# Kernel tuning notes

Hardware: AMD Instinct MI355X
Metric: run time of the kernel (lower is better)

Reference implementation:

```python
import jax, jax.numpy as jnp
import numpy as np

C, CL = 64, 8
N_PTS, GRID = 250_000, 160
G2 = GRID // 2


def _build():
    """Build sparse coords and MinkowskiEngine-style kernel maps (numpy, int constants)."""
    rng = np.random.default_rng(0)
    raw = rng.integers(0, GRID, size=(int(N_PTS * 1.3), 3))
    keys = (raw[:, 0] * GRID + raw[:, 1]) * GRID + raw[:, 2]
    _, uidx = np.unique(keys, return_index=True)
    coords = raw[np.sort(uidx)][:N_PTS]
    n_in = coords.shape[0]
    # conv1: kernel 2, stride 2 -> each input voxel maps to exactly one output via one of 8 offsets
    down = coords // 2
    dkeys = (down[:, 0] * G2 + down[:, 1]) * G2 + down[:, 2]
    ukeys, inv = np.unique(dkeys, return_inverse=True)
    n_out = int(ukeys.shape[0])
    kid = (coords[:, 0] % 2) * 4 + (coords[:, 1] % 2) * 2 + (coords[:, 2] % 2)
    lists = [np.where(kid == k)[0] for k in range(8)]
    M1 = max(len(l) for l in lists)
    in1 = np.full((8, M1), n_in, np.int32)   # pad -> zero feature row
    out1 = np.full((8, M1), n_out, np.int32)  # pad -> dropped output row
    for k, l in enumerate(lists):
        in1[k, :len(l)] = l
        out1[k, :len(l)] = inv[l]
    # kernel-3, stride-1 map on the downsampled coordinate set (27 offsets)
    D = np.stack([ukeys // (G2 * G2), (ukeys // G2) % G2, ukeys % G2], 1)
    offs = [(a, b, c) for a in (-1, 0, 1) for b in (-1, 0, 1) for c in (-1, 0, 1)]
    pin, pout = [], []
    for o in offs:
        nd = D + np.array(o)
        valid = np.all((nd >= 0) & (nd < G2), 1)
        nk = (nd[:, 0] * G2 + nd[:, 1]) * G2 + nd[:, 2]
        pos = np.minimum(np.searchsorted(ukeys, nk), n_out - 1)
        found = valid & (ukeys[pos] == nk)
        ii = np.where(found)[0]
        pin.append(ii)
        pout.append(pos[ii])
    M3 = max(len(p) for p in pin)
    in3 = np.full((27, M3), n_out, np.int32)
    out3 = np.full((27, M3), n_out, np.int32)
    for k in range(27):
        in3[k, :len(pin[k])] = pin[k]
        out3[k, :len(pin[k])] = pout[k]
    return n_in, n_out, in1, out1, in3, out3


def setup_inputs() -> dict:
    n_in, n_out, in1, out1, in3, out3 = _build()
    key = jax.random.key(0)
    ks = jax.random.split(key, 16)
    s = 0.05
    return dict(
        x_F=jax.random.normal(ks[0], (n_in, C), jnp.float32),
        ctx_F=jax.random.normal(ks[1], (n_in, C), jnp.float32),
        W1=jax.random.normal(ks[2], (8, 2 * C, C), jnp.float32) * s,
        b1=jax.random.normal(ks[3], (C,), jnp.float32) * s,
        Wr00=jax.random.normal(ks[4], (27, C, C // 4), jnp.float32) * s,
        br00=jax.random.normal(ks[5], (C // 4,), jnp.float32) * s,
        Wr01=jax.random.normal(ks[6], (27, C // 4, C // 2), jnp.float32) * s,
        br01=jax.random.normal(ks[7], (C // 2,), jnp.float32) * s,
        Wr10=jax.random.normal(ks[8], (C, C // 4), jnp.float32) * s,
        br10=jax.random.normal(ks[9], (C // 4,), jnp.float32) * s,
        Wr11=jax.random.normal(ks[10], (27, C // 4, C // 4), jnp.float32) * s,
        br11=jax.random.normal(ks[11], (C // 4,), jnp.float32) * s,
        Wr12=jax.random.normal(ks[12], (C // 4, C // 2), jnp.float32) * s,
        br12=jax.random.normal(ks[13], (C // 2,), jnp.float32) * s,
        W2=jax.random.normal(ks[14], (27, C, CL), jnp.float32) * s,
        b2=jax.random.normal(ks[15], (CL,), jnp.float32) * s,
        in1=jnp.asarray(in1), out1=jnp.asarray(out1),
        in3=jnp.asarray(in3), out3=jnp.asarray(out3),
        n_out=n_out,
    )


def _sconv(F, W, b, in_idx, out_idx, n_out):
    """Kernel-map sparse conv: per-offset gather -> GEMM -> scatter-add. F:[N,Cin], W:[K,Cin,Cout]."""
    Fp = jnp.concatenate([F, jnp.zeros((1, F.shape[1]), F.dtype)], 0)
    y = jnp.zeros((n_out + 1, W.shape[2]), F.dtype)
    for k in range(W.shape[0]):  # fixed small kernel volume (8 or 27)
        y = y.at[out_idx[k]].add(Fp[in_idx[k]] @ W[k])
    return y[:n_out] + b


def reference(x_F, ctx_F, W1, b1, Wr00, br00, Wr01, br01, Wr10, br10, Wr11, br11, Wr12, br12, W2, b2, in1, out1, in3, out3, n_out):
    relu = jax.nn.relu
    f = jnp.concatenate([x_F, ctx_F], 1)               # cat(x.F, context1.F)
    h = _sconv(f, W1, b1, in1, out1, n_out)            # conv1: 2C->C, k=2, s=2
    # InceptionResNet block (PCGCv2-style)
    out0 = _sconv(relu(_sconv(h, Wr00, br00, in3, out3, n_out)), Wr01, br01, in3, out3, n_out)
    t = relu(h @ Wr10 + br10)                          # 1x1 conv
    t = relu(_sconv(t, Wr11, br11, in3, out3, n_out))  # 3x3 conv
    path1 = t @ Wr12 + br12                            # 1x1 conv
    h = jnp.concatenate([out0, path1], 1) + h          # cat + residual
    return _sconv(h, W2, b2, in3, out3, n_out)         # conv2: C->CL, k=3, s=1
```

## Files before the change

### kernel.cpp

```cpp
#include <hip/hip_runtime.h>

#define DEV __device__ __forceinline__

typedef __attribute__((ext_vector_type(8))) short bf16x8;
typedef __attribute__((ext_vector_type(4))) float f32x4;

DEV float4 ld4(const float* p){ return *reinterpret_cast<const float4*>(p); }

DEV unsigned short f2bf(float f){
    union { float f; unsigned u; } v; v.f = f;
    unsigned r = v.u + 0x7fffu + ((v.u >> 16) & 1u);
    return (unsigned short)(r >> 16);
}
DEV float bf2f(unsigned short s){
    union { unsigned u; float f; } v; v.u = ((unsigned)s) << 16;
    return v.f;
}

DEV void async16(const void* g, void* l){
    __builtin_amdgcn_global_load_lds(
        (const __attribute__((address_space(1))) unsigned*)g,
        (__attribute__((address_space(3))) unsigned*)l, 16, 0, 0);
}

DEV int xcd_swizzle(int orig, int nwg){
    int q = nwg >> 3, r = nwg & 7;
    int x = orig & 7, i = orig >> 3;
    return (x < r ? x*(q+1) : r*(q+1) + (x-r)*q) + i;
}

__global__ __launch_bounds__(256)
void inv_init(int* __restrict__ inv, long n, int defv){
    long i = (long)blockIdx.x*256 + threadIdx.x;
    if (i < n) inv[i] = defv;
}

__global__ __launch_bounds__(256)
void inv_build(const int* __restrict__ inK, const int* __restrict__ outK,
               int* __restrict__ inv, int M, int n_out){
    int k = blockIdx.y;
    int m = blockIdx.x*256 + threadIdx.x;
    if (m >= M) return;
    int o = outK[(long)k*M + m];
    if (o != n_out) inv[(long)k*n_out + o] = inK[(long)k*M + m];
}

__global__ __launch_bounds__(256)
void zero_rows(unsigned short* A, unsigned short* B, unsigned short* C,
               unsigned short* D, unsigned short* E, unsigned short* Z,
               int n_out, int n_in){
    int t = threadIdx.x;
    if (t < 64)       A[(long)n_out*64 + t] = 0;
    else if (t < 80)  B[(long)n_out*16 + (t-64)] = 0;
    else if (t < 144) C[(long)n_out*64 + (t-80)] = 0;
    else if (t < 160) D[(long)n_out*16 + (t-144)] = 0;
    else if (t < 176) E[(long)n_out*16 + (t-160)] = 0;
    else if (t < 240) Z[(long)n_in*64 + (t-176)] = 0;
}

__global__ __launch_bounds__(256)
void wfrag_unpaired(const float* __restrict__ W, unsigned short* __restrict__ F,
                    int KC, int NT, int CIN, int CR, int total){
    int idx = blockIdx.x*256 + threadIdx.x;
    if (idx >= total) return;
    int j = idx & 7, l = (idx >> 3) & 63, rest = idx >> 9;
    int nt = rest % NT, cc = rest / NT;
    int k = cc / KC, kc = cc % KC;
    int g = l >> 4, c = l & 15;
    int cin = kc*32 + g*8 + j, cout = nt*16 + c;
    float v = (cout < CR) ? W[((long)k*CIN + cin)*CR + cout] : 0.f;
    F[idx] = f2bf(v);
}

__global__ __launch_bounds__(256)
void wfrag_paired(const float* __restrict__ W, unsigned short* __restrict__ F,
                  int NKr, int NT, int CR, int total){
    int idx = blockIdx.x*256 + threadIdx.x;
    if (idx >= total) return;
    int j = idx & 7, l = (idx >> 3) & 63, rest = idx >> 9;
    int nt = rest % NT, cc = rest / NT;
    int g = l >> 4, c = l & 15;
    int koff = 2*cc + (g >> 1);
    int cin = (g & 1)*8 + j, cout = nt*16 + c;
    float v = (koff < NKr && cout < CR) ? W[((long)koff*16 + cin)*CR + cout] : 0.f;
    F[idx] = f2bf(v);
}

template<bool RELU, bool OUTBF16, int YS, int CR>
__global__ __launch_bounds__(256)
void gather27_lds(const void* __restrict__ Xv, const unsigned short* __restrict__ Wf,
                  const int* __restrict__ inv, const float* __restrict__ bias,
                  void* __restrict__ Yv, int n_out)
{
    __shared__ alignas(16) char buf[2*16384];
    const int lane = threadIdx.x & 63, w = threadIdx.x >> 6;
    const int bid = xcd_swizzle(blockIdx.x, gridDim.x);
    const long jblock = (long)bid * 64;
    if (jblock >= n_out) return;
    const int r = lane & 15, g = lane >> 4;
    const char* X = (const char*)Xv;
    const bf16x8* __restrict__ WF = (const bf16x8*)Wf;

    const int scol = (((lane & 7) ^ (lane >> 3)) << 4);
    const long jr0 = min(jblock + w*16 +     (lane >> 3), (long)n_out - 1);
    const long jr1 = min(jblock + w*16 + 8 + (lane >> 3), (long)n_out - 1);

    const int ro0 = w*4096 + r*128 + (( 0 + g*16) ^ ((r & 7) << 4));
    const int ro1 = w*4096 + r*128 + ((64 + g*16) ^ ((r & 7) << 4));

    f32x4 acc = {0,0,0,0};

    int i0a = inv[jr0],                 i0b = inv[jr1];
    int i1a = inv[(long)n_out + jr0],   i1b = inv[(long)n_out + jr1];
    {
        char* d = buf + w*4096;
        async16(X + (long)i0a*128 + scol, d);
        async16(X + (long)i0b*128 + scol, d + 1024);
        async16(X + (long)i1a*128 + scol, d + 2048);
        async16(X + (long)i1b*128 + scol, d + 3072);
    }
    int n0a = inv[(long)2*n_out + jr0], n0b = inv[(long)2*n_out + jr1];
    int n1a = inv[(long)3*n_out + jr0], n1b = inv[(long)3*n_out + jr1];
    bf16x8 w00 = WF[0*64 + lane], w01 = WF[1*64 + lane];
    bf16x8 w10 = WF[2*64 + lane], w11 = WF[3*64 + lane];
    __syncthreads();

    #pragma unroll 1
    for (int t = 0; t < 13; ++t){
        const int cb = t & 1;
        {
            char* d = buf + (cb^1)*16384 + w*4096;
            async16(X + (long)n0a*128 + scol, d);
            async16(X + (long)n0b*128 + scol, d + 1024);
            async16(X + (long)n1a*128 + scol, d + 2048);
            async16(X + (long)n1b*128 + scol, d + 3072);
        }
        const long kiA = (long)min(2*t+4, 26) * n_out;
        const long kiB = (long)min(2*t+5, 26) * n_out;
        int t0a = inv[kiA + jr0], t0b = inv[kiA + jr1];
        int t1a = inv[kiB + jr0], t1b = inv[kiB + jr1];
        const long kwA = (long)min(2*t+2, 26) * 2;
        const long kwB = (long)min(2*t+3, 26) * 2;
        bf16x8 nw00 = WF[(kwA  )*64 + lane], nw01 = WF[(kwA+1)*64 + lane];
        bf16x8 nw10 = WF[(kwB  )*64 + lane], nw11 = WF[(kwB+1)*64 + lane];
        const char* base = buf + cb*16384;
        bf16x8 a00 = *(const bf16x8*)(base + ro0);
        bf16x8 a01 = *(const bf16x8*)(base + ro1);
        bf16x8 a10 = *(const bf16x8*)(base + 2048 + ro0);
        bf16x8 a11 = *(const bf16x8*)(base + 2048 + ro1);
        acc = __builtin_amdgcn_mfma_f32_16x16x32_bf16(a00, w00, acc, 0, 0, 0);
        acc = __builtin_amdgcn_mfma_f32_16x16x32_bf16(a01, w01, acc, 0, 0, 0);
        acc = __builtin_amdgcn_mfma_f32_16x16x32_bf16(a10, w10, acc, 0, 0, 0);
        acc = __builtin_amdgcn_mfma_f32_16x16x32_bf16(a11, w11, acc, 0, 0, 0);
        __syncthreads();
        n0a=t0a; n0b=t0b; n1a=t1a; n1b=t1b;
        w00=nw00; w01=nw01; w10=nw10; w11=nw11;
    }
    {
        const char* base = buf + 16384;
        bf16x8 a00 = *(const bf16x8*)(base + ro0);
        bf16x8 a01 = *(const bf16x8*)(base + ro1);
        acc = __builtin_amdgcn_mfma_f32_16x16x32_bf16(a00, w00, acc, 0, 0, 0);
        acc = __builtin_amdgcn_mfma_f32_16x16x32_bf16(a01, w01, acc, 0, 0, 0);
    }

    const float bv = (r < CR) ? bias[r] : 0.f;
    #pragma unroll
    for (int q = 0; q < 4; ++q){
        long row = jblock + w*16 + g*4 + q;
        if (row < n_out){
            float v = acc[q] + bv;
            if constexpr (RELU) v = fmaxf(v, 0.f);
            if constexpr (OUTBF16) ((unsigned short*)Yv)[row*YS + r] = f2bf(v);
            else if (r < CR)       ((float*)Yv)[row*YS + r] = v;
        }
    }
}

__global__ __launch_bounds__(256, 8)
void conv1_z(const float* __restrict__ xF, const float* __restrict__ cF,
             const unsigned short* __restrict__ Wfc1, const int* __restrict__ in1,
             unsigned short* __restrict__ Z, int M1, int n_in)
{
    __shared__ unsigned short tz[4][16*64];
    const int k = blockIdx.x;
    const int lane = threadIdx.x & 63, wave = threadIdx.x >> 6;
    const int m0 = (blockIdx.y*4 + wave)*16;
    if (m0 >= M1) return;
    const int r = lane & 15, g = lane >> 4;
    const int* __restrict__ in1k = in1 + (long)k*M1;
    const int mc = min(m0 + r, M1-1);
    const int i = in1k[mc];
    const bool valid = i < n_in;
    const long iv = valid ? i : 0;
    const bf16x8* __restrict__ WF = (const bf16x8*)(Wfc1 + (size_t)k*16*512);
    const bf16x8 az = {0,0,0,0,0,0,0,0};
    f32x4 acc[4];
    #pragma unroll
    for (int nt=0; nt<4; ++nt) acc[nt] = f32x4{0,0,0,0};

    float4 lo[4], hi[4];
    #pragma unroll
    for (int kc=0; kc<4; ++kc){
        const float* s = (kc < 2) ? (xF + iv*64 + kc*32 + g*8)
                                  : (cF + iv*64 + (kc-2)*32 + g*8);
        lo[kc] = ld4(s);
        hi[kc] = ld4(s+4);
    }
    #pragma unroll
    for (int kc=0; kc<4; ++kc){
        bf16x8 a;
        a[0]=(short)f2bf(lo[kc].x); a[1]=(short)f2bf(lo[kc].y);
        a[2]=(short)f2bf(lo[kc].z); a[3]=(short)f2bf(lo[kc].w);
        a[4]=(short)f2bf(hi[kc].x); a[5]=(short)f2bf(hi[kc].y);
        a[6]=(short)f2bf(hi[kc].z); a[7]=(short)f2bf(hi[kc].w);
        if (!valid) a = az;
        #pragma unroll
        for (int nt=0; nt<4; ++nt){
            bf16x8 wv = WF[((long)kc*4 + nt)*64 + lane];
            acc[nt] = __builtin_amdgcn_mfma_f32_16x16x32_bf16(a, wv, acc[nt], 0, 0, 0);
        }
    }

    #pragma unroll
    for (int q=0; q<4; ++q)
        #pragma unroll
        for (int nt=0; nt<4; ++nt)
            tz[wave][(g*4+q)*64 + nt*16 + r] = f2bf(acc[nt][q]);
    __syncthreads();
    #pragma unroll
    for (int it=0; it<2; ++it){
        int cid = it*64 + lane;
        int row = cid >> 3, c8 = (cid & 7)*8;
        int m = m0 + row;
        if (m < M1){
            int oi = in1k[m];
            long drow = (oi < n_in) ? (long)oi : (long)n_in + 1;
            *(bf16x8*)(Z + drow*64 + c8) = *(const bf16x8*)(&tz[wave][row*64 + c8]);
        }
    }
}

__global__ __launch_bounds__(256)
void conv1_sum(const unsigned short* __restrict__ Z, const int* __restrict__ inv1,
               const float* __restrict__ b1, unsigned short* __restrict__ A, int n_out)
{
    const int bid = xcd_swizzle(blockIdx.x, gridDim.x);
    const long t = (long)bid*256 + threadIdx.x;
    const long o = t >> 3;
    if (o >= n_out) return;
    const int c8 = (int)(t & 7) * 8;
    int b[8];
    #pragma unroll
    for (int k=0;k<8;++k) b[k] = inv1[(long)k*n_out + o];
    float acc[8];
    #pragma unroll
    for (int j=0;j<2;++j){
        float4 v = ld4(b1 + c8 + 4*j);
        acc[4*j]=v.x; acc[4*j+1]=v.y; acc[4*j+2]=v.z; acc[4*j+3]=v.w;
    }
    #pragma unroll
    for (int k=0;k<8;++k){
        bf16x8 z = *(const bf16x8*)(Z + (long)b[k]*64 + c8);
        #pragma unroll
        for (int j=0;j<8;++j) acc[j] += bf2f((unsigned short)z[j]);
    }
    bf16x8 outv;
    #pragma unroll
    for (int j=0;j<8;++j) outv[j] = (short)f2bf(acc[j]);
    *(bf16x8*)(A + o*64 + c8) = outv;
}

template<int NK, int G, int NT, int RB, bool RELU, int RESBASE,
         int YS, int CB, int CR, int WPE>
__global__ __launch_bounds__(256, WPE)
void mfma_g1(const void* __restrict__ Xv, const unsigned short* __restrict__ Wf,
             const int* __restrict__ inv, const float* __restrict__ bias,
             const unsigned short* __restrict__ RES, unsigned short* __restrict__ Y, int n_out)
{
    const int lane = threadIdx.x & 63, wave = threadIdx.x >> 6;
    const int jbase = (blockIdx.x*4 + wave)*32;
    if (jbase >= n_out) return;
    const int r = lane & 15, g = lane >> 4;
    const int jc0 = min(jbase + r, n_out-1), jc1 = min(jbase + 16 + r, n_out-1);
    const char* X = (const char*)Xv;
    const bf16x8* __restrict__ WF = (const bf16x8*)Wf;
    f32x4 acc0[NT], acc1[NT];
    #pragma unroll
    for (int nt=0; nt<NT; ++nt){ acc0[nt] = f32x4{0,0,0,0}; acc1[nt] = f32x4{0,0,0,0}; }

    #pragma unroll 1
    for (int g0 = 0; g0 < NK; g0 += G) {
        int b0[G], b1[G];
        #pragma unroll
        for (int kk=0; kk<G; ++kk){
            int koff = 2*(g0+kk) + (g >> 1);
            b0[kk] = inv[(long)koff*n_out + jc0];
            b1[kk] = inv[(long)koff*n_out + jc1];
        }
        #pragma unroll
        for (int kk=0; kk<G; ++kk){
            const int k = g0 + kk;
            bf16x8 a0 = *(const bf16x8*)(X + (long)b0[kk]*RB + (g&1)*16);
            bf16x8 a1 = *(const bf16x8*)(X + (long)b1[kk]*RB + (g&1)*16);
            #pragma unroll
            for (int nt=0; nt<NT; ++nt){
                bf16x8 wv = WF[((long)k*NT + nt)*64 + lane];
                acc0[nt] = __builtin_amdgcn_mfma_f32_16x16x32_bf16(a0, wv, acc0[nt], 0, 0, 0);
                acc1[nt] = __builtin_amdgcn_mfma_f32_16x16x32_bf16(a1, wv, acc1[nt], 0, 0, 0);
            }
        }
    }

    float bi[NT];
    #pragma unroll
    for (int nt=0; nt<NT; ++nt){
        int c = nt*16 + r;
        bi[nt] = (c < CR) ? bias[c] : 0.f;
    }
    #pragma unroll
    for (int q=0; q<4; ++q){
        int row = jbase + g*4 + q;
        if (row < n_out){
            #pragma unroll
            for (int nt=0; nt<NT; ++nt){
                int c = nt*16 + r;
                float v = acc0[nt][q] + bi[nt];
                if constexpr (RESBASE >= 0) v += bf2f(RES[(long)row*64 + RESBASE + c]);
                if constexpr (RELU) v = fmaxf(v, 0.f);
                Y[(long)row*YS + CB + c] = f2bf(v);
            }
        }
        int row2 = jbase + 16 + g*4 + q;
        if (row2 < n_out){
            #pragma unroll
            for (int nt=0; nt<NT; ++nt){
                int c = nt*16 + r;
                float v = acc1[nt][q] + bi[nt];
                if constexpr (RESBASE >= 0) v += bf2f(RES[(long)row2*64 + RESBASE + c]);
                if constexpr (RELU) v = fmaxf(v, 0.f);
                Y[(long)row2*YS + CB + c] = f2bf(v);
            }
        }
    }
}

template<int MODE, int NT, int RB, bool RELU, int RESBASE, int YS, int CB, int CR>
__global__ __launch_bounds__(256)
void mfma_dense(const void* __restrict__ Xv, const unsigned short* __restrict__ Wf,
                const float* __restrict__ bias, const unsigned short* __restrict__ RES,
                unsigned short* __restrict__ Y, int n_out)
{
    const int lane = threadIdx.x & 63, wave = threadIdx.x >> 6;
    const int jbase = (blockIdx.x*4 + wave)*16;
    if (jbase >= n_out) return;
    const int r = lane & 15, g = lane >> 4;
    const int jrow = jbase + r;
    const bool rowok = jrow < n_out;
    const char* X = (const char*)Xv;
    const bf16x8* __restrict__ WF = (const bf16x8*)Wf;
    const bf16x8 az = {0,0,0,0,0,0,0,0};
    f32x4 acc[NT];
    #pragma unroll
    for (int nt=0; nt<NT; ++nt) acc[nt] = f32x4{0,0,0,0};

    if constexpr (MODE == 2) {
        #pragma unroll
        for (int kc=0; kc<2; ++kc){
            bf16x8 a = az;
            if (rowok) a = *(const bf16x8*)(X + (long)jrow*RB + kc*64 + g*16);
            #pragma unroll
            for (int nt=0; nt<NT; ++nt){
                bf16x8 wv = WF[((long)kc*NT + nt)*64 + lane];
                acc[nt] = __builtin_amdgcn_mfma_f32_16x16x32_bf16(a, wv, acc[nt], 0, 0, 0);
            }
        }
    } else {
        bf16x8 a = az;
        if (rowok && g < 2) a = *(const bf16x8*)(X + (long)jrow*RB + (g&1)*16);
        #pragma unroll
        for (int nt=0; nt<NT; ++nt){
            bf16x8 wv = WF[nt*64 + lane];
            acc[nt] = __builtin_amdgcn_mfma_f32_16x16x32_bf16(a, wv, acc[nt], 0, 0, 0);
        }
    }

    float bi[NT];
    #pragma unroll
    for (int nt=0; nt<NT; ++nt){
        int c = nt*16 + r;
        bi[nt] = (c < CR) ? bias[c] : 0.f;
    }
    #pragma unroll
    for (int q=0; q<4; ++q){
        int row = jbase + g*4 + q;
        if (row < n_out){
            #pragma unroll
            for (int nt=0; nt<NT; ++nt){
                int c = nt*16 + r;
                float v = acc[nt][q] + bi[nt];
                if constexpr (RESBASE >= 0) v += bf2f(RES[(long)row*64 + RESBASE + c]);
                if constexpr (RELU) v = fmaxf(v, 0.f);
                Y[(long)row*YS + CB + c] = f2bf(v);
            }
        }
    }
}

extern "C" void kernel_launch(void* const* d_in, const int* in_sizes, int n_in_cnt,
                              void* d_out, int out_size, void* d_ws, size_t ws_size,
                              hipStream_t stream)
{
    const float* xF   = (const float*)d_in[0];
    const float* ctxF = (const float*)d_in[1];
    const float* W1   = (const float*)d_in[2];
    const float* b1   = (const float*)d_in[3];
    const float* Wr00 = (const float*)d_in[4];
    const float* br00 = (const float*)d_in[5];
    const float* Wr01 = (const float*)d_in[6];
    const float* br01 = (const float*)d_in[7];
    const float* Wr10 = (const float*)d_in[8];
    const float* br10 = (const float*)d_in[9];
    const float* Wr11 = (const float*)d_in[10];
    const float* br11 = (const float*)d_in[11];
    const float* Wr12 = (const float*)d_in[12];
    const float* br12 = (const float*)d_in[13];
    const float* W2   = (const float*)d_in[14];
    const float* b2   = (const float*)d_in[15];
    const int* in1  = (const int*)d_in[16];
    const int* out1 = (const int*)d_in[17];
    const int* in3  = (const int*)d_in[18];
    const int* out3 = (const int*)d_in[19];

    const int n_out = out_size / 8;
    const int n_in  = in_sizes[0] / 64;
    const int M1 = in_sizes[16] / 8;
    const int M3 = in_sizes[18] / 27;

    char* p = (char*)d_ws;
    int* inv3 = (int*)p;                 p += (size_t)28*n_out*4;
    int* inv1 = (int*)p;                 p += (size_t)8*n_out*4;
    unsigned short* A = (unsigned short*)p;  p += (size_t)(n_out+1)*64*2;
    unsigned short* B = (unsigned short*)p;  p += (size_t)(n_out+1)*16*2;
    unsigned short* C = (unsigned short*)p;  p += (size_t)(n_out+1)*64*2;
    unsigned short* D = (unsigned short*)p;  p += (size_t)(n_out+1)*16*2;
    unsigned short* E = (unsigned short*)p;  p += (size_t)(n_out+1)*16*2;
    unsigned short* Z = (unsigned short*)p;  p += (size_t)(n_in+2)*64*2;
    unsigned short* Wf_c1 = (unsigned short*)p;  p += (size_t)32*4*512*2;
    unsigned short* Wf_00 = (unsigned short*)p;  p += (size_t)54*512*2;
    unsigned short* Wf_2  = (unsigned short*)p;  p += (size_t)54*512*2;
    unsigned short* Wf_01 = (unsigned short*)p;  p += (size_t)14*2*512*2;
    unsigned short* Wf_11 = (unsigned short*)p;  p += (size_t)14*512*2;
    unsigned short* Wf_10 = (unsigned short*)p;  p += (size_t)2*512*2;
    unsigned short* Wf_12 = (unsigned short*)p;  p += (size_t)2*512*2;
    float* OUT = (float*)d_out;

    auto cdiv = [](long a, long b){ return (int)((a + b - 1)/b); };

    inv_init<<<cdiv((long)28*n_out,256),256,0,stream>>>(inv3, (long)28*n_out, n_out);
    inv_init<<<cdiv((long)8*n_out,256),256,0,stream>>>(inv1, (long)8*n_out, n_in);
    inv_build<<<dim3(cdiv(M3,256),27),256,0,stream>>>(in3, out3, inv3, M3, n_out);
    inv_build<<<dim3(cdiv(M1,256),8),256,0,stream>>>(in1, out1, inv1, M1, n_out);
    zero_rows<<<1,256,0,stream>>>(A, B, C, D, E, Z, n_out, n_in);

    wfrag_unpaired<<<cdiv(32*4*512,256),256,0,stream>>>(W1,   Wf_c1, 4, 4, 128, 64, 32*4*512);
    wfrag_unpaired<<<cdiv(54*512,256),  256,0,stream>>>(Wr00, Wf_00, 2, 1,  64, 16, 54*512);
    wfrag_unpaired<<<cdiv(54*512,256),  256,0,stream>>>(W2,   Wf_2,  2, 1,  64,  8, 54*512);
    wfrag_unpaired<<<cdiv(2*512,256),   256,0,stream>>>(Wr10, Wf_10, 2, 1,  64, 16, 2*512);
    wfrag_paired  <<<cdiv(14*2*512,256),256,0,stream>>>(Wr01, Wf_01, 27, 2, 32, 14*2*512);
    wfrag_paired  <<<cdiv(14*512,256),  256,0,stream>>>(Wr11, Wf_11, 27, 1, 16, 14*512);
    wfrag_paired  <<<cdiv(2*512,256),   256,0,stream>>>(Wr12, Wf_12,  1, 2, 32, 2*512);

    conv1_z<<<dim3(8,cdiv(M1,64)),256,0,stream>>>(xF, ctxF, Wf_c1, in1, Z, M1, n_in);
    conv1_sum<<<cdiv((long)8*n_out,256),256,0,stream>>>(Z, inv1, b1, A, n_out);

    const int grid_g = cdiv(n_out, 128);
    const int grid_l = cdiv(n_out, 64);
    const int grid_d = cdiv(n_out, 64);

    gather27_lds<true, true, 16, 16>
        <<<grid_l,256,0,stream>>>(A, Wf_00, inv3, br00, B, n_out);
    mfma_dense<2, 1, 128, true, -1, 16, 0, 16>
        <<<grid_d,256,0,stream>>>(A, Wf_10, br10, nullptr, D, n_out);
    mfma_g1<14,7,2, 32, false, 0, 64, 0, 32, 4>
        <<<grid_g,256,0,stream>>>(B, Wf_01, inv3, br01, A, C, n_out);
    mfma_g1<14,7,1, 32, true, -1, 16, 0, 16, 4>
        <<<grid_g,256,0,stream>>>(D, Wf_11, inv3, br11, nullptr, E, n_out);
    mfma_dense<3, 2, 32, false, 32, 64, 32, 32>
        <<<grid_d,256,0,stream>>>(E, Wf_12, br12, A, C, n_out);
    gather27_lds<false, false, 8, 8>
        <<<grid_l,256,0,stream>>>(C, Wf_2, inv3, b2, OUT, n_out);
}
```

Measured before the change: 273.3 us.

## Replace async LDS gathers with register-staged wave-private double buffering

The 27-offset gather-GEMM kernel no longer uses global_load_lds async copies staged two offsets at a time with block-wide barriers. Each wave now gathers one offset per iteration into registers, runs the MFMAs on the previous buffer, then writes the gathered rows to its own half of a smaller double buffer. There are no __syncthreads, because each wave reads and writes only its own LDS region. The intent is to remove barrier stalls and halve LDS use so more blocks fit per CU. The cost is a shallower prefetch, so global load latency is covered only by one iteration of MFMA work, plus extra VGPRs to hold the staged data.

Measured after the change: 263.6 us. -3.5%, faster.

```diff
diff --git a/kernel.cpp b/kernel.cpp
--- a/kernel.cpp
+++ b/kernel.cpp
@@ -15,12 +15,6 @@
 DEV float bf2f(unsigned short s){
     union { unsigned u; float f; } v; v.u = ((unsigned)s) << 16;
     return v.f;
-}
-
-DEV void async16(const void* g, void* l){
-    __builtin_amdgcn_global_load_lds(
-        (const __attribute__((address_space(1))) unsigned*)g,
-        (__attribute__((address_space(3))) unsigned*)l, 16, 0, 0);
 }
 
 DEV int xcd_swizzle(int orig, int nwg){
@@ -92,7 +86,7 @@
                   const int* __restrict__ inv, const float* __restrict__ bias,
                   void* __restrict__ Yv, int n_out)
 {
-    __shared__ alignas(16) char buf[2*16384];
+    __shared__ alignas(16) char buf[2*8192];
     const int lane = threadIdx.x & 63, w = threadIdx.x >> 6;
     const int bid = xcd_swizzle(blockIdx.x, gridDim.x);
     const long jblock = (long)bid * 64;
@@ -101,67 +95,52 @@
     const char* X = (const char*)Xv;
     const bf16x8* __restrict__ WF = (const bf16x8*)Wf;
 
-    const int scol = (((lane & 7) ^ (lane >> 3)) << 4);
-    const long jr0 = min(jblock + w*16 +     (lane >> 3), (long)n_out - 1);
-    const long jr1 = min(jblock + w*16 + 8 + (lane >> 3), (long)n_out - 1);
-
-    const int ro0 = w*4096 + r*128 + (( 0 + g*16) ^ ((r & 7) << 4));
-    const int ro1 = w*4096 + r*128 + ((64 + g*16) ^ ((r & 7) << 4));
+    const int srow = lane >> 3;
+    const int scol = (lane & 7) << 4;
+    const long jr0 = min(jblock + w*16 + srow,     (long)n_out - 1);
+    const long jr1 = min(jblock + w*16 + 8 + srow, (long)n_out - 1);
+    const int wo0 = w*2048 + srow*128     + (scol ^ (srow << 4));
+    const int wo1 = w*2048 + (8+srow)*128 + (scol ^ (srow << 4));
+    const int ro0 = w*2048 + r*128 + ((     g*16) ^ ((r & 7) << 4));
+    const int ro1 = w*2048 + r*128 + ((64 + g*16) ^ ((r & 7) << 4));
 
     f32x4 acc = {0,0,0,0};
 
-    int i0a = inv[jr0],                 i0b = inv[jr1];
-    int i1a = inv[(long)n_out + jr0],   i1b = inv[(long)n_out + jr1];
-    {
-        char* d = buf + w*4096;
-        async16(X + (long)i0a*128 + scol, d);
-        async16(X + (long)i0b*128 + scol, d + 1024);
-        async16(X + (long)i1a*128 + scol, d + 2048);
-        async16(X + (long)i1b*128 + scol, d + 3072);
-    }
-    int n0a = inv[(long)2*n_out + jr0], n0b = inv[(long)2*n_out + jr1];
-    int n1a = inv[(long)3*n_out + jr0], n1b = inv[(long)3*n_out + jr1];
-    bf16x8 w00 = WF[0*64 + lane], w01 = WF[1*64 + lane];
-    bf16x8 w10 = WF[2*64 + lane], w11 = WF[3*64 + lane];
-    __syncthreads();
+    int i0 = inv[jr0], i1 = inv[jr1];
+    float4 f0 = ld4((const float*)(X + (long)i0*128 + scol));
+    float4 f1 = ld4((const float*)(X + (long)i1*128 + scol));
+    int n0 = inv[(long)n_out + jr0], n1 = inv[(long)n_out + jr1];
+    bf16x8 wc0 = WF[lane], wc1 = WF[64 + lane];
+    *(float4*)(buf + wo0) = f0;
+    *(float4*)(buf + wo1) = f1;
 
     #pragma unroll 1
-    for (int t = 0; t < 13; ++t){
-        const int cb = t & 1;
-        {
-            char* d = buf + (cb^1)*16384 + w*4096;
-            async16(X + (long)n0a*128 + scol, d);
-            async16(X + (long)n0b*128 + scol, d + 1024);
-            async16(X + (long)n1a*128 + scol, d + 2048);
-            async16(X + (long)n1b*128 + scol, d + 3072);
-        }
-        const long kiA = (long)min(2*t+4, 26) * n_out;
-        const long kiB = (long)min(2*t+5, 26) * n_out;
-        int t0a = inv[kiA + jr0], t0b = inv[kiA + jr1];
-        int t1a = inv[kiB + jr0], t1b = inv[kiB + jr1];
-        const long kwA = (long)min(2*t+2, 26) * 2;
-        const long kwB = (long)min(2*t+3, 26) * 2;
-        bf16x8 nw00 = WF[(kwA  )*64 + lane], nw01 = WF[(kwA+1)*64 + lane];
-        bf16x8 nw10 = WF[(kwB  )*64 + lane], nw11 = WF[(kwB+1)*64 + lane];
-        const char* base = buf + cb*16384;
-        bf16x8 a00 = *(const bf16x8*)(base + ro0);
-        bf16x8 a01 = *(const bf16x8*)(base + ro1);
-        bf16x8 a10 = *(const bf16x8*)(base + 2048 + ro0);
-        bf16x8 a11 = *(const bf16x8*)(base + 2048 + ro1);
-        acc = __builtin_amdgcn_mfma_f32_16x16x32_bf16(a00, w00, acc, 0, 0, 0);
-        acc = __builtin_amdgcn_mfma_f32_16x16x32_bf16(a01, w01, acc, 0, 0, 0);
-        acc = __builtin_amdgcn_mfma_f32_16x16x32_bf16(a10, w10, acc, 0, 0, 0);
-        acc = __builtin_amdgcn_mfma_f32_16x16x32_bf16(a11, w11, acc, 0, 0, 0);
-        __syncthreads();
-        n0a=t0a; n0b=t0b; n1a=t1a; n1b=t1b;
-        w00=nw00; w01=nw01; w10=nw10; w11=nw11;
-    }
-    {
-        const char* base = buf + 16384;
-        bf16x8 a00 = *(const bf16x8*)(base + ro0);
-        bf16x8 a01 = *(const bf16x8*)(base + ro1);
-        acc = __builtin_amdgcn_mfma_f32_16x16x32_bf16(a00, w00, acc, 0, 0, 0);
-        acc = __builtin_amdgcn_mfma_f32_16x16x32_bf16(a01, w01, acc, 0, 0, 0);
+    for (int k = 0; k < 27; ++k){
+        const int cb = k & 1;
+        float4 g0, g1;
+        if (k < 26){
+            g0 = ld4((const float*)(X + (long)n0*128 + scol));
+            g1 = ld4((const float*)(X + (long)n1*128 + scol));
+        }
+        int t0 = 0, t1 = 0;
+        if (k < 25){
+            const long ko = (long)(k+2)*n_out;
+            t0 = inv[ko + jr0]; t1 = inv[ko + jr1];
+        }
+        bf16x8 wn0 = wc0, wn1 = wc1;
+        if (k < 26){
+            wn0 = WF[((long)(k+1)*2    )*64 + lane];
+            wn1 = WF[((long)(k+1)*2 + 1)*64 + lane];
+        }
+        bf16x8 a0 = *(const bf16x8*)(buf + cb*8192 + ro0);
+        bf16x8 a1 = *(const bf16x8*)(buf + cb*8192 + ro1);
+        acc = __builtin_amdgcn_mfma_f32_16x16x32_bf16(a0, wc0, acc, 0, 0, 0);
+        acc = __builtin_amdgcn_mfma_f32_16x16x32_bf16(a1, wc1, acc, 0, 0, 0);
+        if (k < 26){
+            *(float4*)(buf + (cb^1)*8192 + wo0) = g0;
+            *(float4*)(buf + (cb^1)*8192 + wo1) = g1;
+        }
+        n0 = t0; n1 = t1; wc0 = wn0; wc1 = wn1;
     }
 
     const float bv = (r < CR) ? bias[r] : 0.f;
```
